# Performance work log

Measured on AMD Instinct MI355X. Metric: run time of the kernel, lower is better.

## Reference

```python
import jax, jax.numpy as jnp
import numpy as np

NUM_HEADS = 3
DIM = 96
MLP_HIDDEN = int(DIM * 4.0)
LN_EPS = 1e-5


def _layernorm(x, g, b):
    mu = jnp.mean(x, axis=-1, keepdims=True)
    var = jnp.mean(jnp.square(x - mu), axis=-1, keepdims=True)
    return (x - mu) * jax.lax.rsqrt(var + LN_EPS) * g + b


def setup_inputs() -> dict:
    key = jax.random.key(0)
    ks = jax.random.split(key, 12)
    B, H, W, T, C = 1, 48, 48, 48, DIM
    L = H * W * T
    s = 0.02
    return {
        "x": jax.random.normal(ks[0], (B, L, C), dtype=jnp.float32),
        "mask_matrix": jnp.zeros((1, 1), dtype=jnp.float32),
        "ln1_g": jnp.ones((C,), jnp.float32),
        "ln1_b": jnp.zeros((C,), jnp.float32),
        "qkv_w": jax.random.normal(ks[1], (3 * C, C), jnp.float32) * s,
        "qkv_b": jnp.zeros((3 * C,), jnp.float32),
        "proj_w": jax.random.normal(ks[2], (C, C), jnp.float32) * s,
        "proj_b": jnp.zeros((C,), jnp.float32),
        "ln2_g": jnp.ones((C,), jnp.float32),
        "ln2_b": jnp.zeros((C,), jnp.float32),
        "fc1_w": jax.random.normal(ks[3], (MLP_HIDDEN, C), jnp.float32) * s,
        "fc1_b": jnp.zeros((MLP_HIDDEN,), jnp.float32),
        "fc2_w": jax.random.normal(ks[4], (C, MLP_HIDDEN), jnp.float32) * s,
        "fc2_b": jnp.zeros((C,), jnp.float32),
        "H": 48, "W": 48, "T": 48,
    }


def reference(x, mask_matrix, ln1_g, ln1_b, qkv_w, qkv_b, proj_w, proj_b,
              ln2_g, ln2_b, fc1_w, fc1_b, fc2_w, fc2_b, H, W, T):
    B, L, C = x.shape
    nh = NUM_HEADS
    hd = C // nh
    scale = hd ** -0.5

    shortcut = x
    h = _layernorm(x, ln1_g, ln1_b)
    # [B,H,W,T,C] -> permute(0,3,1,2,4) -> [B*T, H*W, C]  (axial_dims='12', extra_dim=3)
    h = h.reshape(B, H, W, T, C).transpose(0, 3, 1, 2, 4).reshape(B * T, H * W, C)
    B_, N, _ = h.shape

    qkv = h @ qkv_w.T + qkv_b                       # [B_, N, 3C]
    # faithful to torch: permute(1,0,2) -> reshape(1,N,3,nh,B_*hd) -> permute(2,0,3,1,4)
    qkv = jnp.transpose(qkv, (1, 0, 2)).reshape(1, N, 3, nh, B_ * hd)
    qkv = jnp.transpose(qkv, (2, 0, 3, 1, 4))       # [3, 1, nh, N, B_*hd]
    q, k, v = qkv[0] * scale, qkv[1], qkv[2]

    attn = jax.nn.softmax(q @ jnp.swapaxes(k, -2, -1), axis=-1)  # [1, nh, N, N]
    o = attn @ v                                    # [1, nh, N, B_*hd]
    o = jnp.transpose(o, (0, 2, 1, 3)).reshape(B_, N, C)
    o = o @ proj_w.T + proj_b
    # faithful to torch: plain view back to [B, H*W*T, C] (no inverse permute)
    o = o.reshape(B, H * W * T, C)

    x = shortcut + o
    h2 = _layernorm(x, ln2_g, ln2_b)
    m = jax.nn.gelu(h2 @ fc1_w.T + fc1_b, approximate=False) @ fc2_w.T + fc2_b
    return x + m
```

## Files before the change

kernel.cpp:

```cpp
#include <hip/hip_runtime.h>
#include <hip/hip_bf16.h>
#include <math.h>

typedef __bf16 bf16_t;
typedef __bf16 bf16x8 __attribute__((ext_vector_type(8)));
typedef __bf16 bf16x4 __attribute__((ext_vector_type(4)));
typedef float f32x4 __attribute__((ext_vector_type(4)));

#define AS1q __attribute__((address_space(1)))
#define AS3q __attribute__((address_space(3)))

__device__ __forceinline__ void gload_lds16(const bf16_t* g, bf16_t* l) {
    __builtin_amdgcn_global_load_lds((AS1q void*)g, (AS3q void*)l, 16, 0, 0);
}

#define LROWS   110592
#define CDIM    96
#define NTOK    2304
#define FDIM    1536
#define YSTR    3538944ll
#define SSTR    5308416ll
#define SCALE_Q 0.1767766952966369f

__device__ __forceinline__ float gelu_f(float v) {
    float xs = v * 0.70710678118654752f;
    float a  = fabsf(xs);
    float t  = __builtin_amdgcn_rcpf(fmaf(0.3275911f, a, 1.0f));
    float p  = t * fmaf(t, fmaf(t, fmaf(t, fmaf(t, 1.061405429f, -1.453152027f),
                                        1.421413741f), -0.284496736f), 0.254829592f);
    float e  = __expf(-a * a);
    float erfx = copysignf(fmaf(-p, e, 1.0f), xs);
    return 0.5f * v * (1.0f + erfx);
}

__global__ __launch_bounds__(256)
void conv_w(const float* __restrict__ a, const float* __restrict__ b,
            const float* __restrict__ c, const float* __restrict__ d,
            bf16_t* __restrict__ out)
{
    int i = blockIdx.x * 256 + threadIdx.x;
    float v;
    if (i < 27648)       v = a[i];
    else if (i < 36864)  v = b[i - 27648];
    else if (i < 73728)  v = c[i - 36864];
    else                 v = d[i - 73728];
    out[i] = (bf16_t)v;
}

__global__ __launch_bounds__(256)
void softmax_k(const bf16_t* __restrict__ S, bf16_t* __restrict__ P,
               long long sZ, long long pZ)
{
    int wv = threadIdx.x >> 6, lane = threadIdx.x & 63;
    int row = blockIdx.x * 4 + wv;
    const bf16_t* sr = S + (size_t)blockIdx.z * sZ + (size_t)row * NTOK;
    bf16_t* pr = P + (size_t)blockIdx.z * pZ + (size_t)row * NTOK;
    float v[36];
    float mx = -1e30f;
    #pragma unroll
    for (int t = 0; t < 9; t++) {
        bf16x4 c = *(const bf16x4*)(sr + (size_t)(t * 64 + lane) * 4);
        #pragma unroll
        for (int j = 0; j < 4; j++) { v[t*4+j] = (float)c[j]; mx = fmaxf(mx, v[t*4+j]); }
    }
    #pragma unroll
    for (int off = 32; off > 0; off >>= 1) mx = fmaxf(mx, __shfl_xor(mx, off, 64));
    float sum = 0.f;
    #pragma unroll
    for (int j = 0; j < 36; j++) { v[j] = __expf(v[j] - mx); sum += v[j]; }
    #pragma unroll
    for (int off = 32; off > 0; off >>= 1) sum += __shfl_xor(sum, off, 64);
    float inv = 1.f / sum;
    #pragma unroll
    for (int t = 0; t < 9; t++) {
        bf16x4 o;
        #pragma unroll
        for (int j = 0; j < 4; j++) o[j] = (bf16_t)(v[t*4+j] * inv);
        *(bf16x4*)(pr + (size_t)(t * 64 + lane) * 4) = o;
    }
}

template<int BN, int EPI, int NBY>
__global__ __launch_bounds__(256, 2)
void gemm_bt(const bf16_t* __restrict__ A, const bf16_t* __restrict__ W,
             void* __restrict__ out, int K,
             long long aZ, long long wZ, long long oZ, float scale)
{
    constexpr int BM = 128, BK = 64;
    constexpr int MI = 4;
    constexpr int NT = BN / 32;
    constexpr int NB = 18 * NBY;
    constexpr int CHK = (NB + 7) / 8;
    __shared__ bf16_t As[BM * BK];
    __shared__ bf16_t Bs[BN * BK];

    int id = blockIdx.x;
    int id2 = (id & 7) * CHK + (id >> 3);
    if (id2 >= NB) return;
    int p  = id2 / 108;
    int r_ = id2 - p * 108;
    int by = p * 6 + (r_ % 6);
    int bx = r_ / 6;

    const int tid = threadIdx.x;
    const int wave = tid >> 6, lane = tid & 63;
    const int quad = lane >> 4, l16 = lane & 15;
    const int wm = wave & 1, wn = wave >> 1;
    const int z = blockIdx.z;
    A += (size_t)z * aZ;
    W += (size_t)z * wZ;
    const int m0 = bx * BM, n0 = by * BN;

    f32x4 acc[MI][NT];
    #pragma unroll
    for (int i = 0; i < MI; i++)
        #pragma unroll
        for (int j = 0; j < NT; j++) { f32x4 zz = {0.f, 0.f, 0.f, 0.f}; acc[i][j] = zz; }

    const int srow = lane >> 3;
    const int scol = lane & 7;

    constexpr int NA = BM / 32;
    constexpr int NBC = BN / 32;
    const bf16_t* pa[NA]; bf16_t* la[NA];
    #pragma unroll
    for (int t = 0; t < NA; t++) {
        int it = t * 4 + wave;
        int r = it * 8 + srow;
        int cg = scol ^ (r & 7);
        pa[t] = A + (size_t)(m0 + r) * K + cg * 8;
        la[t] = &As[it * 512];
    }
    const bf16_t* pb[NBC]; bf16_t* lb[NBC];
    #pragma unroll
    for (int t = 0; t < NBC; t++) {
        int it = t * 4 + wave;
        int r = it * 8 + srow;
        int cg = scol ^ (r & 7);
        pb[t] = W + (size_t)(n0 + r) * K + cg * 8;
        lb[t] = &Bs[it * 512];
    }

    for (int k0 = 0; k0 < K; k0 += BK) {
        __syncthreads();
        #pragma unroll
        for (int t = 0; t < NA; t++)  gload_lds16(pa[t] + k0, la[t]);
        #pragma unroll
        for (int t = 0; t < NBC; t++) gload_lds16(pb[t] + k0, lb[t]);
        __syncthreads();

        bf16x8 af[MI][2], bfr[NT][2];
        #pragma unroll
        for (int i = 0; i < MI; i++) {
            int r = wm * 64 + i * 16 + l16;
            #pragma unroll
            for (int kk = 0; kk < 2; kk++)
                af[i][kk] = *(const bf16x8*)&As[r * 64 + (((kk * 4 + quad) ^ (r & 7)) << 3)];
        }
        #pragma unroll
        for (int j = 0; j < NT; j++) {
            int c = wn * (BN / 2) + j * 16 + l16;
            #pragma unroll
            for (int kk = 0; kk < 2; kk++)
                bfr[j][kk] = *(const bf16x8*)&Bs[c * 64 + (((kk * 4 + quad) ^ (c & 7)) << 3)];
        }
        #pragma unroll
        for (int kk = 0; kk < 2; kk++)
            #pragma unroll
            for (int i = 0; i < MI; i++)
                #pragma unroll
                for (int j = 0; j < NT; j++)
                    acc[i][j] = __builtin_amdgcn_mfma_f32_16x16x32_bf16(af[i][kk], bfr[j][kk], acc[i][j], 0, 0, 0);
    }

    #pragma unroll
    for (int i = 0; i < MI; i++)
        #pragma unroll
        for (int j = 0; j < NT; j++)
            #pragma unroll
            for (int ri = 0; ri < 4; ri++) {
                int r = m0 + wm * 64 + i * 16 + quad * 4 + ri;
                int c = n0 + wn * (BN / 2) + j * 16 + l16;
                float v = acc[i][j][ri];
                if constexpr (EPI == 1) {
                    bf16_t* op = (bf16_t*)out + (size_t)z * oZ;
                    op[(size_t)r * NTOK + c] = (bf16_t)(v * scale);
                } else {
                    int b = r / 48, rr = r - b * 48;
                    ((bf16_t*)out)[((size_t)(b * NTOK + rr * 48 + z * 16)) * CDIM + c] = (bf16_t)v;
                }
            }
}

__global__ __launch_bounds__(256, 2)
void qkv_fused(const float* __restrict__ X, const bf16_t* __restrict__ Wg,
               bf16_t* __restrict__ out, const float* __restrict__ bias,
               bf16_t* __restrict__ outv,
               const float* __restrict__ g1, const float* __restrict__ b1)
{
    constexpr int N = 288, K = 96;
    constexpr int KP = K + 8;
    constexpr int NT = N / 16;
    constexpr int KI = K / 32;
    __shared__ __attribute__((aligned(16))) bf16_t Ws[N * KP];

    const int tid = threadIdx.x;
    const int wave = tid >> 6, lane = tid & 63;
    const int quad = lane >> 4, l16 = lane & 15;
    const int m0 = blockIdx.x * 256;

    constexpr int CH = N * K / 8;
    for (int c = tid; c < CH; c += 256) {
        int row = c / (K / 8), kc = c - row * (K / 8);
        bf16x8 w = *(const bf16x8*)(Wg + row * K + kc * 8);
        *(bf16x8*)(Ws + row * KP + kc * 8) = w;
    }
    __syncthreads();

    const int t = m0 / NTOK;
    const int nb = m0 - t * NTOK;

    f32x4 gv[KI][2], bv[KI][2];
    #pragma unroll
    for (int kk = 0; kk < KI; kk++) {
        const float* gp = g1 + quad * 8 + kk * 32;
        const float* bp = b1 + quad * 8 + kk * 32;
        gv[kk][0] = *(const f32x4*)gp;     gv[kk][1] = *(const f32x4*)(gp + 4);
        bv[kk][0] = *(const f32x4*)bp;     bv[kk][1] = *(const f32x4*)(bp + 4);
    }

    bf16x8 af[4][KI];
    #pragma unroll
    for (int i = 0; i < 4; i++) {
        size_t l = (size_t)(nb + wave * 64 + l16 + i * 16) * 48 + t;
        const float* xr = X + l * 96 + quad * 8;
        f32x4 xv[KI][2];
        float s1 = 0.f, s2 = 0.f;
        #pragma unroll
        for (int kk = 0; kk < KI; kk++) {
            xv[kk][0] = *(const f32x4*)(xr + kk * 32);
            xv[kk][1] = *(const f32x4*)(xr + kk * 32 + 4);
            #pragma unroll
            for (int h = 0; h < 2; h++)
                #pragma unroll
                for (int j = 0; j < 4; j++) {
                    float v = xv[kk][h][j];
                    s1 += v; s2 += v * v;
                }
        }
        s1 += __shfl_xor(s1, 16, 64);  s1 += __shfl_xor(s1, 32, 64);
        s2 += __shfl_xor(s2, 16, 64);  s2 += __shfl_xor(s2, 32, 64);
        float mean = s1 * (1.f / 96.f);
        float var  = s2 * (1.f / 96.f) - mean * mean;
        float rstd = rsqrtf(var + 1e-5f);
        #pragma unroll
        for (int kk = 0; kk < KI; kk++)
            #pragma unroll
            for (int h = 0; h < 2; h++)
                #pragma unroll
                for (int j = 0; j < 4; j++)
                    af[i][kk][h * 4 + j] =
                        (bf16_t)((xv[kk][h][j] - mean) * rstd * gv[kk][h][j] + bv[kk][h][j]);
    }

    #pragma unroll 2
    for (int nt = 0; nt < NT; nt++) {
        bf16x8 bfr[KI];
        #pragma unroll
        for (int kk = 0; kk < KI; kk++)
            bfr[kk] = *(const bf16x8*)(Ws + (nt * 16 + l16) * KP + kk * 32 + quad * 8);
        f32x4 a4[4];
        #pragma unroll
        for (int i = 0; i < 4; i++) { f32x4 zz = {0.f, 0.f, 0.f, 0.f}; a4[i] = zz; }
        #pragma unroll
        for (int kk = 0; kk < KI; kk++)
            #pragma unroll
            for (int i = 0; i < 4; i++)
                a4[i] = __builtin_amdgcn_mfma_f32_16x16x32_bf16(af[i][kk], bfr[kk], a4[i], 0, 0, 0);

        int c = nt * 16 + l16;
        int jj = t * 288 + c;
        int g = jj / FDIM, mm = jj - g * FDIM;
        float bvv = bias[c];
        if (g < 6) {
            bf16_t* yp = out + (size_t)g * YSTR + mm;
            #pragma unroll
            for (int i = 0; i < 4; i++)
                #pragma unroll
                for (int ri = 0; ri < 4; ri++) {
                    int n = nb + wave * 64 + i * 16 + quad * 4 + ri;
                    yp[(size_t)n * FDIM] = (bf16_t)(a4[i][ri] + bvv);
                }
        } else {
            bf16_t* vp = outv + (size_t)(g - 6) * YSTR + (size_t)mm * NTOK;
            #pragma unroll
            for (int i = 0; i < 4; i++) {
                int n0q = nb + wave * 64 + i * 16 + quad * 4;
                bf16x4 o;
                #pragma unroll
                for (int ri = 0; ri < 4; ri++) o[ri] = (bf16_t)(a4[i][ri] + bvv);
                *(bf16x4*)(vp + n0q) = o;
            }
        }
    }
}

template<int N, int K, int KC, int EPI>
__global__ __launch_bounds__(256, 2)
void gemm_ws(const bf16_t* __restrict__ A, const bf16_t* __restrict__ Wg,
             void* __restrict__ out, const float* __restrict__ bias,
             const float* __restrict__ resid,
             bf16_t* __restrict__ out2, const float* __restrict__ g2,
             const float* __restrict__ b2)
{
    constexpr int KP = K + 8;
    constexpr int NT = N / 16;
    constexpr int KI = KC / 32;
    __shared__ __attribute__((aligned(16))) bf16_t Ws[N * KP];

    const int tid = threadIdx.x;
    const int wave = tid >> 6, lane = tid & 63;
    const int quad = lane >> 4, l16 = lane & 15;
    const int m0 = blockIdx.x * 256;

    constexpr int CH = N * K / 8;
    for (int c = tid; c < CH; c += 256) {
        int row = c / (K / 8), kc = c - row * (K / 8);
        bf16x8 w = *(const bf16x8*)(Wg + row * K + kc * 8);
        *(bf16x8*)(Ws + row * KP + kc * 8) = w;
    }
    __syncthreads();

    const bf16_t* Ar = A + (size_t)(m0 + wave * 64 + l16) * K + quad * 8;

    f32x4 acc[4][NT];
    #pragma unroll
    for (int i = 0; i < 4; i++)
        #pragma unroll
        for (int j = 0; j < NT; j++) { f32x4 zz = {0.f, 0.f, 0.f, 0.f}; acc[i][j] = zz; }
    for (int kc0 = 0; kc0 < K; kc0 += KC) {
        bf16x8 af[4][KI];
        #pragma unroll
        for (int i = 0; i < 4; i++)
            #pragma unroll
            for (int kk = 0; kk < KI; kk++)
                af[i][kk] = *(const bf16x8*)(Ar + (size_t)i * 16 * K + kc0 + kk * 32);
        #pragma unroll
        for (int nt = 0; nt < NT; nt++) {
            #pragma unroll
            for (int kk = 0; kk < KI; kk++) {
                bf16x8 b = *(const bf16x8*)(Ws + (nt * 16 + l16) * KP + kc0 + kk * 32 + quad * 8);
                #pragma unroll
                for (int i = 0; i < 4; i++)
                    acc[i][nt] = __builtin_amdgcn_mfma_f32_16x16x32_bf16(af[i][kk], b, acc[i][nt], 0, 0, 0);
            }
        }
    }
    if constexpr (EPI == 5) {
        float bv[NT], gv[NT], bb[NT];
        #pragma unroll
        for (int nt = 0; nt < NT; nt++) {
            int c = nt * 16 + l16;
            bv[nt] = bias[c]; gv[nt] = g2[c]; bb[nt] = b2[c];
        }
        #pragma unroll
        for (int i = 0; i < 4; i++)
            #pragma unroll
            for (int ri = 0; ri < 4; ri++) {
                int r = m0 + wave * 64 + i * 16 + quad * 4 + ri;
                float u[NT];
                float s = 0.f;
                #pragma unroll
                for (int nt = 0; nt < NT; nt++) {
                    int c = nt * 16 + l16;
                    u[nt] = acc[i][nt][ri] + bv[nt] + resid[(size_t)r * N + c];
                    ((float*)out)[(size_t)r * N + c] = u[nt];
                    s += u[nt];
                }
                #pragma unroll
                for (int off = 8; off > 0; off >>= 1) s += __shfl_xor(s, off, 64);
                float mean = s * (1.f / 96.f);
                float vs = 0.f;
                #pragma unroll
                for (int nt = 0; nt < NT; nt++) {
                    float dd = u[nt] - mean;
                    u[nt] = dd;
                    vs += dd * dd;
                }
                #pragma unroll
                for (int off = 8; off > 0; off >>= 1) vs += __shfl_xor(vs, off, 64);
                float rstd = rsqrtf(vs * (1.f / 96.f) + 1e-5f);
                #pragma unroll
                for (int nt = 0; nt < NT; nt++) {
                    int c = nt * 16 + l16;
                    out2[(size_t)r * N + c] = (bf16_t)(u[nt] * rstd * gv[nt] + bb[nt]);
                }
            }
    }
}

__global__ __launch_bounds__(256, 4)
void mlp_fused(const bf16_t* __restrict__ A, const bf16_t* __restrict__ W1g,
               const bf16_t* __restrict__ W2g, const float* __restrict__ b1,
               const float* __restrict__ b2, const float* __restrict__ resid,
               float* __restrict__ out)
{
    constexpr int KP1 = 104;
    constexpr int TBS = 44;
    __shared__ __attribute__((aligned(16))) bf16_t W1c[2][32 * KP1];
    __shared__ __attribute__((aligned(16))) bf16_t W2c[2][96 * 40];
    __shared__ __attribute__((aligned(16))) bf16_t Tb[128 * TBS];

    const int tid = threadIdx.x;
    const int wave = tid >> 6, lane = tid & 63;
    const int quad = lane >> 4, l16 = lane & 15;
    const int m0 = blockIdx.x * 128;

    const bf16_t* Ar = A + (size_t)(m0 + wave * 32 + l16) * 96 + quad * 8;
    bf16x8 af[2][3];
    #pragma unroll
    for (int i = 0; i < 2; i++)
        #pragma unroll
        for (int kk = 0; kk < 3; kk++)
            af[i][kk] = *(const bf16x8*)(Ar + (size_t)i * 16 * 96 + kk * 32);

    bf16x4 w1n[3], w2n[3];
    #pragma unroll
    for (int q = 0; q < 3; q++) {
        int e = q * 256 + tid;
        w1n[q] = *(const bf16x4*)(W1g + e * 4);
        int row = e >> 3, sub = e & 7;
        w2n[q] = *(const bf16x4*)(W2g + row * 384 + sub * 4);
    }
    #pragma unroll
    for (int q = 0; q < 3; q++) {
        int e = q * 256 + tid;
        int r1 = e / 24, s1 = e - r1 * 24;
        *(bf16x4*)(&W1c[0][r1 * KP1 + s1 * 4]) = w1n[q];
        int row = e >> 3, sub = e & 7;
        *(bf16x4*)(&W2c[0][row * 40 + sub * 4]) = w2n[q];
    }
    __syncthreads();

    f32x4 acc2[2][6];
    #pragma unroll
    for (int i = 0; i < 2; i++)
        #pragma unroll
        for (int j = 0; j < 6; j++) { f32x4 zz = {0.f, 0.f, 0.f, 0.f}; acc2[i][j] = zz; }

    for (int c = 0; c < 12; c++) {
        const int pb = c & 1;
        if (c < 11) {
            #pragma unroll
            for (int q = 0; q < 3; q++) {
                int e = q * 256 + tid;
                w1n[q] = *(const bf16x4*)(W1g + (c + 1) * 3072 + e * 4);
                int row = e >> 3, sub = e & 7;
                w2n[q] = *(const bf16x4*)(W2g + row * 384 + (c + 1) * 32 + sub * 4);
            }
        }
        f32x4 a1[2][2];
        #pragma unroll
        for (int i = 0; i < 2; i++)
            #pragma unroll
            for (int s = 0; s < 2; s++) { f32x4 zz = {0.f, 0.f, 0.f, 0.f}; a1[i][s] = zz; }
        #pragma unroll
        for (int s = 0; s < 2; s++) {
            int n = s * 16 + l16;
            #pragma unroll
            for (int kk = 0; kk < 3; kk++) {
                bf16x8 b = *(const bf16x8*)(&W1c[pb][n * KP1 + kk * 32 + quad * 8]);
                #pragma unroll
                for (int i = 0; i < 2; i++)
                    a1[i][s] = __builtin_amdgcn_mfma_f32_16x16x32_bf16(af[i][kk], b, a1[i][s], 0, 0, 0);
            }
        }
        #pragma unroll
        for (int s = 0; s < 2; s++) {
            int n = c * 32 + s * 16 + l16;
            float bv = b1[n];
            #pragma unroll
            for (int i = 0; i < 2; i++)
                #pragma unroll
                for (int ri = 0; ri < 4; ri++) {
                    float u = gelu_f(a1[i][s][ri] + bv);
                    Tb[(wave * 32 + i * 16 + quad * 4 + ri) * TBS + s * 16 + l16] = (bf16_t)u;
                }
        }
        if (c < 11) {
            #pragma unroll
            for (int q = 0; q < 3; q++) {
                int e = q * 256 + tid;
                int r1 = e / 24, s1 = e - r1 * 24;
                *(bf16x4*)(&W1c[pb ^ 1][r1 * KP1 + s1 * 4]) = w1n[q];
                int row = e >> 3, sub = e & 7;
                *(bf16x4*)(&W2c[pb ^ 1][row * 40 + sub * 4]) = w2n[q];
            }
        }
        bf16x8 a2[2];
        #pragma unroll
        for (int i = 0; i < 2; i++) {
            const bf16_t* tp = Tb + (wave * 32 + i * 16 + l16) * TBS + quad * 8;
            bf16x4 lo = *(const bf16x4*)tp;
            bf16x4 hi = *(const bf16x4*)(tp + 4);
            #pragma unroll
            for (int j = 0; j < 4; j++) { a2[i][j] = lo[j]; a2[i][j + 4] = hi[j]; }
        }
        #pragma unroll
        for (int nt = 0; nt < 6; nt++) {
            bf16x8 b = *(const bf16x8*)(&W2c[pb][(nt * 16 + l16) * 40 + quad * 8]);
            #pragma unroll
            for (int i = 0; i < 2; i++)
                acc2[i][nt] = __builtin_amdgcn_mfma_f32_16x16x32_bf16(a2[i], b, acc2[i][nt], 0, 0, 0);
        }
        __syncthreads();
    }

    #pragma unroll
    for (int i = 0; i < 2; i++)
        #pragma unroll
        for (int nt = 0; nt < 6; nt++)
            #pragma unroll
            for (int ri = 0; ri < 4; ri++) {
                int r = m0 + wave * 32 + i * 16 + quad * 4 + ri;
                int cc = nt * 16 + l16;
                out[(size_t)r * 96 + cc] = acc2[i][nt][ri] + b2[cc] + resid[(size_t)r * 96 + cc];
            }
}

extern "C" void kernel_launch(void* const* d_in, const int* in_sizes, int n_in,
                              void* d_out, int out_size, void* d_ws, size_t ws_size,
                              hipStream_t stream)
{
    const float* x      = (const float*)d_in[0];
    const float* ln1_g  = (const float*)d_in[2];
    const float* ln1_b  = (const float*)d_in[3];
    const float* qkv_w  = (const float*)d_in[4];
    const float* qkv_b  = (const float*)d_in[5];
    const float* proj_w = (const float*)d_in[6];
    const float* proj_b = (const float*)d_in[7];
    const float* ln2_g  = (const float*)d_in[8];
    const float* ln2_b  = (const float*)d_in[9];
    const float* fc1_w  = (const float*)d_in[10];
    const float* fc1_b  = (const float*)d_in[11];
    const float* fc2_w  = (const float*)d_in[12];
    const float* fc2_b  = (const float*)d_in[13];

    const size_t SZ_WB = 110592ull * 2;
    const size_t SZ_HP = 10616832ull * 2;
    const size_t SZ_Y  = 31850496ull * 2;
    const size_t SZ_YV = 10616832ull * 2;

    char* ws = (char*)d_ws;
    size_t oWB = 0;
    size_t oHP = oWB + SZ_WB;
    size_t oY  = oHP + SZ_HP;
    size_t oYV = oY + SZ_Y;
    size_t oS  = oYV + SZ_YV;

    bf16_t* Wb    = (bf16_t*)(ws + oWB);
    bf16_t* Wqkv  = Wb;
    bf16_t* Wproj = Wb + 27648;
    bf16_t* Wfc1  = Wb + 36864;
    bf16_t* Wfc2  = Wb + 73728;
    bf16_t* hp    = (bf16_t*)(ws + oHP);
    bf16_t* Y     = (bf16_t*)(ws + oY);
    bf16_t* Yv    = (bf16_t*)(ws + oYV);
    bf16_t* Pb    = (bf16_t*)(ws + oY);
    bf16_t* Sb    = (bf16_t*)(ws + oS);
    float*  x2    = (float*)(ws + oS);
    float*  outp  = (float*)d_out;

    dim3 blk(256);

    conv_w<<<dim3(432), blk, 0, stream>>>(qkv_w, proj_w, fc1_w, fc2_w, Wb);
    qkv_fused<<<dim3(432), blk, 0, stream>>>(x, Wqkv, Y, qkv_b, Yv, ln1_g, ln1_b);
    gemm_bt<128, 1, 18><<<dim3(328, 1, 3), blk, 0, stream>>>(Y, Y + 3 * YSTR, Sb,
                                                             1536, YSTR, YSTR, SSTR, SCALE_Q);
    softmax_k<<<dim3(576, 1, 3), blk, 0, stream>>>(Sb, Pb, SSTR, SSTR);
    gemm_bt<128, 2, 12><<<dim3(216, 1, 3), blk, 0, stream>>>(Pb, Yv, hp,
                                                             2304, SSTR, YSTR, 0, 0.f);
    gemm_ws<96, 96, 96, 5><<<dim3(432), blk, 0, stream>>>(hp, Wproj, x2, proj_b, x,
                                                          hp, ln2_g, ln2_b);
    mlp_fused<<<dim3(864), blk, 0, stream>>>(hp, Wfc1, Wfc2, fc1_b, fc2_b, x2, outp);
}
```

Baseline: 323.9 us.

## Replace attention GEMMs with 256x256 double-buffered 8-wave pipelined kernel

Replaces the 128-tile single-buffered GEMM used for QK^T and PV with a 512-thread kernel computing 256x256 tiles. The A and B operands are double-buffered in LDS and the next tiles are prefetched while MFMAs run, with explicit vmcnt waits, barriers and setprio. Work groups are remapped across XCDs. The aim is more data reuse per tile and hiding global-load latency behind compute, at the cost of 128KB of LDS, one block per CU and fewer blocks (81 and 54 per head) to fill the GPU.

```diff
diff --git a/kernel.cpp b/kernel.cpp
--- a/kernel.cpp
+++ b/kernel.cpp
@@ -80,107 +80,147 @@
     }
 }
 
-template<int BN, int EPI, int NBY>
-__global__ __launch_bounds__(256, 2)
-void gemm_bt(const bf16_t* __restrict__ A, const bf16_t* __restrict__ W,
-             void* __restrict__ out, int K,
-             long long aZ, long long wZ, long long oZ, float scale)
+template<int EPI>
+__global__ __launch_bounds__(512, 1)
+void gemm_bt8(const bf16_t* __restrict__ A, const bf16_t* __restrict__ W,
+              void* __restrict__ out, int K,
+              long long aZ, long long wZ, long long oZ, float scale)
 {
-    constexpr int BM = 128, BK = 64;
-    constexpr int MI = 4;
-    constexpr int NT = BN / 32;
-    constexpr int NB = 18 * NBY;
-    constexpr int CHK = (NB + 7) / 8;
-    __shared__ bf16_t As[BM * BK];
-    __shared__ bf16_t Bs[BN * BK];
-
-    int id = blockIdx.x;
-    int id2 = (id & 7) * CHK + (id >> 3);
-    if (id2 >= NB) return;
-    int p  = id2 / 108;
-    int r_ = id2 - p * 108;
-    int by = p * 6 + (r_ % 6);
-    int bx = r_ / 6;
+    constexpr int BK = 64;
+    __shared__ __attribute__((aligned(16))) bf16_t LA[2][2][128 * 64];
+    __shared__ __attribute__((aligned(16))) bf16_t LB[2][2][128 * 64];
+
+    const int nb = gridDim.x;
+    const int orig = blockIdx.x;
+    const int q8 = nb >> 3, r8 = nb & 7;
+    const int xcd = orig & 7;
+    const int wgid = (xcd < r8 ? xcd * (q8 + 1) : r8 * (q8 + 1) + (xcd - r8) * q8)
+                   + (orig >> 3);
+    const int bx = wgid % 9;
+    const int by = wgid / 9;
 
     const int tid = threadIdx.x;
     const int wave = tid >> 6, lane = tid & 63;
     const int quad = lane >> 4, l16 = lane & 15;
-    const int wm = wave & 1, wn = wave >> 1;
+    const int wm = wave >> 2, wn = wave & 3;
     const int z = blockIdx.z;
     A += (size_t)z * aZ;
     W += (size_t)z * wZ;
-    const int m0 = bx * BM, n0 = by * BN;
-
-    f32x4 acc[MI][NT];
-    #pragma unroll
-    for (int i = 0; i < MI; i++)
-        #pragma unroll
-        for (int j = 0; j < NT; j++) { f32x4 zz = {0.f, 0.f, 0.f, 0.f}; acc[i][j] = zz; }
+    const int m0 = bx * 256, n0 = by * 256;
+
+    f32x4 acc[8][4];
+    #pragma unroll
+    for (int i = 0; i < 8; i++)
+        #pragma unroll
+        for (int j = 0; j < 4; j++) { f32x4 zz = {0.f, 0.f, 0.f, 0.f}; acc[i][j] = zz; }
 
     const int srow = lane >> 3;
     const int scol = lane & 7;
 
-    constexpr int NA = BM / 32;
-    constexpr int NBC = BN / 32;
-    const bf16_t* pa[NA]; bf16_t* la[NA];
-    #pragma unroll
-    for (int t = 0; t < NA; t++) {
-        int it = t * 4 + wave;
-        int r = it * 8 + srow;
-        int cg = scol ^ (r & 7);
-        pa[t] = A + (size_t)(m0 + r) * K + cg * 8;
-        la[t] = &As[it * 512];
-    }
-    const bf16_t* pb[NBC]; bf16_t* lb[NBC];
-    #pragma unroll
-    for (int t = 0; t < NBC; t++) {
-        int it = t * 4 + wave;
-        int r = it * 8 + srow;
-        int cg = scol ^ (r & 7);
-        pb[t] = W + (size_t)(n0 + r) * K + cg * 8;
-        lb[t] = &Bs[it * 512];
-    }
-
-    for (int k0 = 0; k0 < K; k0 += BK) {
-        __syncthreads();
-        #pragma unroll
-        for (int t = 0; t < NA; t++)  gload_lds16(pa[t] + k0, la[t]);
-        #pragma unroll
-        for (int t = 0; t < NBC; t++) gload_lds16(pb[t] + k0, lb[t]);
-        __syncthreads();
-
-        bf16x8 af[MI][2], bfr[NT][2];
-        #pragma unroll
-        for (int i = 0; i < MI; i++) {
-            int r = wm * 64 + i * 16 + l16;
+    auto stageA = [&](int buf, int h, int kt) {
+        #pragma unroll
+        for (int s = 0; s < 2; s++) {
+            int it = s * 8 + wave;
+            int r = it * 8 + srow;
+            int cg = scol ^ (r & 7);
+            gload_lds16(A + (size_t)(m0 + h * 128 + r) * K + kt * BK + cg * 8,
+                        &LA[buf][h][it * 512]);
+        }
+    };
+    auto stageB = [&](int buf, int h, int kt) {
+        #pragma unroll
+        for (int s = 0; s < 2; s++) {
+            int it = s * 8 + wave;
+            int r = it * 8 + srow;
+            int cg = scol ^ (r & 7);
+            gload_lds16(W + (size_t)(n0 + h * 128 + r) * K + kt * BK + cg * 8,
+                        &LB[buf][h][it * 512]);
+        }
+    };
+
+    const int bslot = wn >> 1, bcol0 = (wn & 1) * 64;
+    bf16x8 afr[4][2], bfr[2][2];
+
+    auto ldA = [&](int buf, int rh) {
+        #pragma unroll
+        for (int i = 0; i < 4; i++) {
+            int lr = rh * 64 + i * 16 + l16;
             #pragma unroll
             for (int kk = 0; kk < 2; kk++)
-                af[i][kk] = *(const bf16x8*)&As[r * 64 + (((kk * 4 + quad) ^ (r & 7)) << 3)];
-        }
-        #pragma unroll
-        for (int j = 0; j < NT; j++) {
-            int c = wn * (BN / 2) + j * 16 + l16;
+                afr[i][kk] = *(const bf16x8*)&LA[buf][wm][lr * 64 + (((kk * 4 + quad) ^ (lr & 7)) << 3)];
+        }
+    };
+    auto ldB = [&](int buf, int ch) {
+        #pragma unroll
+        for (int j = 0; j < 2; j++) {
+            int lc = bcol0 + ch * 32 + j * 16 + l16;
             #pragma unroll
             for (int kk = 0; kk < 2; kk++)
-                bfr[j][kk] = *(const bf16x8*)&Bs[c * 64 + (((kk * 4 + quad) ^ (c & 7)) << 3)];
-        }
+                bfr[j][kk] = *(const bf16x8*)&LB[buf][bslot][lc * 64 + (((kk * 4 + quad) ^ (lc & 7)) << 3)];
+        }
+    };
+    auto mfma16 = [&](int rh, int ch) {
+        asm volatile("s_waitcnt lgkmcnt(0)" ::: "memory");
+        __builtin_amdgcn_sched_barrier(0);
+        __builtin_amdgcn_s_setprio(1);
         #pragma unroll
         for (int kk = 0; kk < 2; kk++)
             #pragma unroll
-            for (int i = 0; i < MI; i++)
-                #pragma unroll
-                for (int j = 0; j < NT; j++)
-                    acc[i][j] = __builtin_amdgcn_mfma_f32_16x16x32_bf16(af[i][kk], bfr[j][kk], acc[i][j], 0, 0, 0);
-    }
-
-    #pragma unroll
-    for (int i = 0; i < MI; i++)
-        #pragma unroll
-        for (int j = 0; j < NT; j++)
+            for (int i = 0; i < 4; i++)
+                #pragma unroll
+                for (int j = 0; j < 2; j++)
+                    acc[rh * 4 + i][ch * 2 + j] = __builtin_amdgcn_mfma_f32_16x16x32_bf16(
+                        afr[i][kk], bfr[j][kk], acc[rh * 4 + i][ch * 2 + j], 0, 0, 0);
+        __builtin_amdgcn_s_setprio(0);
+    };
+    auto bar = [&] {
+        __builtin_amdgcn_sched_barrier(0);
+        __builtin_amdgcn_s_barrier();
+        __builtin_amdgcn_sched_barrier(0);
+    };
+
+    const int nt = K / BK;
+
+    stageA(0, 0, 0); stageA(0, 1, 0);
+    stageB(0, 0, 0); stageB(0, 1, 0);
+    stageA(1, 0, 1); stageA(1, 1, 1);
+    asm volatile("s_waitcnt vmcnt(4)" ::: "memory");
+    bar();
+
+    for (int t = 0; t < nt; t++) {
+        const int cb = t & 1;
+        ldA(cb, 0); ldB(cb, 0);
+        if (t + 1 < nt) { stageB(cb ^ 1, 0, t + 1); stageB(cb ^ 1, 1, t + 1); }
+        bar();
+        mfma16(0, 0);
+        bar();
+        ldB(cb, 1);
+        bar();
+        mfma16(0, 1);
+        bar();
+        ldA(cb, 1);
+        bar();
+        mfma16(1, 1);
+        bar();
+        ldB(cb, 0);
+        if (t + 2 < nt) { stageA(cb, 0, t + 2); stageA(cb, 1, t + 2); }
+        bar();
+        mfma16(1, 0);
+        if (t < nt - 1) {
+            if (t == nt - 2) asm volatile("s_waitcnt vmcnt(0)" ::: "memory");
+            else             asm volatile("s_waitcnt vmcnt(4)" ::: "memory");
+        }
+        bar();
+    }
+
+    #pragma unroll
+    for (int i = 0; i < 8; i++)
+        #pragma unroll
+        for (int j = 0; j < 4; j++)
             #pragma unroll
             for (int ri = 0; ri < 4; ri++) {
-                int r = m0 + wm * 64 + i * 16 + quad * 4 + ri;
-                int c = n0 + wn * (BN / 2) + j * 16 + l16;
+                int r = m0 + wm * 128 + i * 16 + quad * 4 + ri;
+                int c = n0 + wn * 64 + j * 16 + l16;
                 float v = acc[i][j][ri];
                 if constexpr (EPI == 1) {
                     bf16_t* op = (bf16_t*)out + (size_t)z * oZ;
@@ -575,11 +615,11 @@
 
     conv_w<<<dim3(432), blk, 0, stream>>>(qkv_w, proj_w, fc1_w, fc2_w, Wb);
     qkv_fused<<<dim3(432), blk, 0, stream>>>(x, Wqkv, Y, qkv_b, Yv, ln1_g, ln1_b);
-    gemm_bt<128, 1, 18><<<dim3(328, 1, 3), blk, 0, stream>>>(Y, Y + 3 * YSTR, Sb,
-                                                             1536, YSTR, YSTR, SSTR, SCALE_Q);
+    gemm_bt8<1><<<dim3(81, 1, 3), dim3(512), 0, stream>>>(Y, Y + 3 * YSTR, Sb,
+                                                          1536, YSTR, YSTR, SSTR, SCALE_Q);
     softmax_k<<<dim3(576, 1, 3), blk, 0, stream>>>(Sb, Pb, SSTR, SSTR);
-    gemm_bt<128, 2, 12><<<dim3(216, 1, 3), blk, 0, stream>>>(Pb, Yv, hp,
-                                                             2304, SSTR, YSTR, 0, 0.f);
+    gemm_bt8<2><<<dim3(54, 1, 3), dim3(512), 0, stream>>>(Pb, Yv, hp,
+                                                          2304, SSTR, YSTR, 0, 0.f);
     gemm_ws<96, 96, 96, 5><<<dim3(432), blk, 0, stream>>>(hp, Wproj, x2, proj_b, x,
                                                           hp, ln2_g, ln2_b);
     mlp_fused<<<dim3(864), blk, 0, stream>>>(hp, Wfc1, Wfc2, fc1_b, fc2_b, x2, outp);
```

Result: slower. 348.2 us (+7.5%).
